# Kernel tuning notes

Measured on AMD Instinct MI355X. Metric: run time of the kernel, lower is better.

## Reference

```python
import jax, jax.numpy as jnp
import numpy as np

EPS = 1e-5


def _bn(x, gamma, beta, mean, var):
    # Inference-mode BatchNorm2d over channel dim (NCHW -> axis 1).
    inv = gamma / jnp.sqrt(var + EPS)
    return x * inv[None, :, None, None] + (beta - mean * inv)[None, :, None, None]


def setup_inputs() -> dict:
    key = jax.random.key(0)
    ks = jax.random.split(key, 6)
    N, Cin, Cout, T, V = 64, 64, 128, 300, 25
    x = jax.random.normal(ks[0], (N, Cin, T, V), dtype=jnp.float32)
    A = jax.random.uniform(ks[1], (V, V), dtype=jnp.float32)  # fixed adjacency (non-trainable buffer)
    edge = jnp.ones((V, V), dtype=jnp.float32)                # learnable edge mask, init ones
    gcn_w = jax.random.normal(ks[2], (Cout, Cin), dtype=jnp.float32) * 0.05
    gcn_b = jnp.zeros((Cout,), dtype=jnp.float32)
    res_w = jax.random.normal(ks[3], (Cout, Cin), dtype=jnp.float32) * 0.05
    res_b = jnp.zeros((Cout,), dtype=jnp.float32)
    return {
        'x': x, 'A': A, 'edge': edge,
        'gcn_w': gcn_w, 'gcn_b': gcn_b,
        'bn_gamma': jnp.ones((Cout,), jnp.float32), 'bn_beta': jnp.zeros((Cout,), jnp.float32),
        'bn_mean': jnp.zeros((Cout,), jnp.float32), 'bn_var': jnp.ones((Cout,), jnp.float32),
        'res_w': res_w, 'res_b': res_b,
        'rbn_gamma': jnp.ones((Cout,), jnp.float32), 'rbn_beta': jnp.zeros((Cout,), jnp.float32),
        'rbn_mean': jnp.zeros((Cout,), jnp.float32), 'rbn_var': jnp.ones((Cout,), jnp.float32),
    }


def reference(x, A, edge, gcn_w, gcn_b, bn_gamma, bn_beta, bn_mean, bn_var,
              res_w, res_b, rbn_gamma, rbn_beta, rbn_mean, rbn_var):
    # x: [N, Cin, T, V]
    # residual branch: 1x1 conv + BN (in_channel != out_channel path)
    res = jnp.einsum('oc,nctv->notv', res_w, x) + res_b[None, :, None, None]
    res = _bn(res, rbn_gamma, rbn_beta, rbn_mean, rbn_var)
    # main branch: 1x1 conv -> adjacency einsum -> BN
    y = jnp.einsum('oc,nctv->notv', gcn_w, x) + gcn_b[None, :, None, None]
    y = jnp.einsum('nctv,vw->nctw', y, A * edge)
    y = _bn(y, bn_gamma, bn_beta, bn_mean, bn_var)
    # keep_prob = 1.0 -> Randomized_DropBlock_Ske / DropBlockT_1d are identity
    return jax.nn.relu(y + res)
```

## Files before the change

kernel.cpp:

```cpp
#include <hip/hip_runtime.h>
#include <stdint.h>

#define N_ 64
#define C_ 64
#define O_ 128
#define T_ 300
#define V_ 25
#define TB 4
#define JB (TB * 32)
#define KB 128
#define LDB 136

typedef __attribute__((ext_vector_type(8))) short short8;
typedef __attribute__((ext_vector_type(4))) float floatx4;

__device__ __forceinline__ short f2bf(float f) {
  unsigned u = __float_as_uint(f);
  unsigned r = (u + 0x7FFFu + ((u >> 16) & 1u)) >> 16;
  return (short)(r & 0xFFFFu);
}

__global__ void sgc_prep(const float* __restrict__ A, const float* __restrict__ edge,
                         const float* __restrict__ gcn_w, const float* __restrict__ gcn_b,
                         const float* __restrict__ bn_g, const float* __restrict__ bn_b,
                         const float* __restrict__ bn_m, const float* __restrict__ bn_v,
                         const float* __restrict__ res_w, const float* __restrict__ res_b,
                         const float* __restrict__ rg, const float* __restrict__ rb,
                         const float* __restrict__ rm, const float* __restrict__ rv,
                         short* __restrict__ Wcat, float* __restrict__ M2p,
                         float* __restrict__ Cwp) {
  const int tid = threadIdx.x;
  for (int i = tid; i < 25 * 32; i += 256) {
    const int v = i >> 5, w = i & 31;
    M2p[i] = (w < 25) ? A[v * 25 + w] * edge[v * 25 + w] : 0.f;
  }
  for (int i = tid; i < O_ * 32; i += 256) {
    const int o = i >> 5, w = i & 31;
    const float inv1 = bn_g[o] * rsqrtf(bn_v[o] + 1e-5f);
    const float inv2 = rg[o] * rsqrtf(rv[o] + 1e-5f);
    float S = 0.f;
    if (w < 25) {
      for (int v = 0; v < 25; ++v) S += A[v * 25 + w] * edge[v * 25 + w];
    }
    Cwp[i] = inv1 * gcn_b[o] * S + (bn_b[o] - bn_m[o] * inv1) + inv2 * res_b[o] +
             (rb[o] - rm[o] * inv2);
  }
  for (int i = tid; i < O_ * KB; i += 256) {
    const int o = i >> 7, k = i & 127;
    const float inv1 = bn_g[o] * rsqrtf(bn_v[o] + 1e-5f);
    const float inv2 = rg[o] * rsqrtf(rv[o] + 1e-5f);
    const float val = (k < 64) ? inv2 * res_w[o * 64 + k] : inv1 * gcn_w[o * 64 + (k - 64)];
    Wcat[i] = f2bf(val);
  }
}

__global__ __launch_bounds__(256, 2) void sgc_main(const float* __restrict__ x,
                                                   const short* __restrict__ Wcat,
                                                   const float* __restrict__ M2p,
                                                   const float* __restrict__ Cw,
                                                   float* __restrict__ out) {
  __shared__ short Bs[JB * LDB];
  const int tid = threadIdx.x;
  const int b = blockIdx.x;
  const int n = b / 75;
  const int t0 = (b % 75) * TB;

  {
    const int tl = tid >> 6;
    const int c = tid & 63;
    const float* xrow = x + (((n * C_ + c) * T_) + (t0 + tl)) * V_;
    float xr[25];
#pragma unroll
    for (int v = 0; v < 25; ++v) xr[v] = xrow[v];
#pragma unroll
    for (int v = 0; v < 25; ++v) Bs[(tl * 32 + v) * LDB + c] = f2bf(xr[v]);
#pragma unroll
    for (int v = 25; v < 32; ++v) {
      Bs[(tl * 32 + v) * LDB + c] = 0;
      Bs[(tl * 32 + v) * LDB + 64 + c] = 0;
    }
    float xa[25];
#pragma unroll
    for (int w = 0; w < 25; ++w) xa[w] = 0.f;
    for (int v = 0; v < 25; ++v) {
      const float xv = xr[v];
      const float* m2 = M2p + v * 32;
#pragma unroll
      for (int w = 0; w < 25; ++w) xa[w] = __builtin_fmaf(xv, m2[w], xa[w]);
    }
#pragma unroll
    for (int w = 0; w < 25; ++w) Bs[(tl * 32 + w) * LDB + 64 + c] = f2bf(xa[w]);
  }
  __syncthreads();

  const int lane = tid & 63;
  const int wv = tid >> 6;
  const int l15 = lane & 15;
  const int quad = lane >> 4;
  const int obase = wv * 32;

  short8 af[2][4];
#pragma unroll
  for (int mt = 0; mt < 2; ++mt) {
#pragma unroll
    for (int kq = 0; kq < 4; ++kq) {
      af[mt][kq] =
          *(const short8*)(Wcat + (obase + mt * 16 + l15) * KB + kq * 32 + quad * 8);
    }
  }

  floatx4 acc[2][8];
#pragma unroll
  for (int mt = 0; mt < 2; ++mt)
#pragma unroll
    for (int jt = 0; jt < 8; ++jt) acc[mt][jt] = (floatx4){0.f, 0.f, 0.f, 0.f};

#pragma unroll
  for (int jt = 0; jt < 8; ++jt) {
#pragma unroll
    for (int kq = 0; kq < 4; ++kq) {
      const short8 bf =
          *(const short8*)(&Bs[(jt * 16 + l15) * LDB + kq * 32 + quad * 8]);
      acc[0][jt] = __builtin_amdgcn_mfma_f32_16x16x32_bf16(af[0][kq], bf, acc[0][jt], 0, 0, 0);
      acc[1][jt] = __builtin_amdgcn_mfma_f32_16x16x32_bf16(af[1][kq], bf, acc[1][jt], 0, 0, 0);
    }
  }

#pragma unroll
  for (int mt = 0; mt < 2; ++mt) {
#pragma unroll
    for (int jt = 0; jt < 8; ++jt) {
      const int j = jt * 16 + l15;
      const int w = j & 31;
      if (w < 25) {
        const int tloc = j >> 5;
        const int o0 = obase + mt * 16 + quad * 4;
        float* op = out + (((n * O_ + o0) * T_) + (t0 + tloc)) * V_ + w;
        const float* cwp = Cw + o0 * 32 + w;
#pragma unroll
        for (int r = 0; r < 4; ++r) {
          const float val = acc[mt][jt][r] + cwp[r * 32];
          op[r * (T_ * V_)] = val > 0.f ? val : 0.f;
        }
      }
    }
  }
}

extern "C" void kernel_launch(void* const* d_in, const int* in_sizes, int n_in,
                              void* d_out, int out_size, void* d_ws, size_t ws_size,
                              hipStream_t stream) {
  const float* x = (const float*)d_in[0];
  const float* A = (const float*)d_in[1];
  const float* edge = (const float*)d_in[2];
  const float* gcn_w = (const float*)d_in[3];
  const float* gcn_b = (const float*)d_in[4];
  const float* bn_g = (const float*)d_in[5];
  const float* bn_b = (const float*)d_in[6];
  const float* bn_m = (const float*)d_in[7];
  const float* bn_v = (const float*)d_in[8];
  const float* res_w = (const float*)d_in[9];
  const float* res_b = (const float*)d_in[10];
  const float* rg = (const float*)d_in[11];
  const float* rb = (const float*)d_in[12];
  const float* rm = (const float*)d_in[13];
  const float* rv = (const float*)d_in[14];

  char* ws = (char*)d_ws;
  short* Wcat = (short*)(ws);
  float* M2p = (float*)(ws + 32768);
  float* Cwp = (float*)(ws + 36864);
  float* out = (float*)d_out;

  hipLaunchKernelGGL(sgc_prep, dim3(1), dim3(256), 0, stream, A, edge, gcn_w, gcn_b,
                     bn_g, bn_b, bn_m, bn_v, res_w, res_b, rg, rb, rm, rv, Wcat, M2p, Cwp);
  hipLaunchKernelGGL(sgc_main, dim3(N_ * (T_ / TB)), dim3(256), 0, stream, x, Wcat, M2p,
                     Cwp, out);
}
```

Measured before the change: 475.0 us.

## Stage x loads and output stores through LDS for coalesced vector access

```diff
diff --git a/kernel.cpp b/kernel.cpp
--- a/kernel.cpp
+++ b/kernel.cpp
@@ -10,6 +10,10 @@
 #define JB (TB * 32)
 #define KB 128
 #define LDB 136
+#define SXS 65
+#define BS_OFF 26000
+#define SMEM_BYTES (BS_OFF + JB * LDB * 2)
+#define STW 3200
 
 typedef __attribute__((ext_vector_type(8))) short short8;
 typedef __attribute__((ext_vector_type(4))) float floatx4;
@@ -59,40 +63,14 @@
                                                    const float* __restrict__ M2p,
                                                    const float* __restrict__ Cw,
                                                    float* __restrict__ out) {
-  __shared__ short Bs[JB * LDB];
+  __shared__ __align__(16) char smem[SMEM_BYTES];
+  float* const xs = (float*)smem;
+  short* const Bs = (short*)(smem + BS_OFF);
+
   const int tid = threadIdx.x;
   const int b = blockIdx.x;
   const int n = b / 75;
   const int t0 = (b % 75) * TB;
-
-  {
-    const int tl = tid >> 6;
-    const int c = tid & 63;
-    const float* xrow = x + (((n * C_ + c) * T_) + (t0 + tl)) * V_;
-    float xr[25];
-#pragma unroll
-    for (int v = 0; v < 25; ++v) xr[v] = xrow[v];
-#pragma unroll
-    for (int v = 0; v < 25; ++v) Bs[(tl * 32 + v) * LDB + c] = f2bf(xr[v]);
-#pragma unroll
-    for (int v = 25; v < 32; ++v) {
-      Bs[(tl * 32 + v) * LDB + c] = 0;
-      Bs[(tl * 32 + v) * LDB + 64 + c] = 0;
-    }
-    float xa[25];
-#pragma unroll
-    for (int w = 0; w < 25; ++w) xa[w] = 0.f;
-    for (int v = 0; v < 25; ++v) {
-      const float xv = xr[v];
-      const float* m2 = M2p + v * 32;
-#pragma unroll
-      for (int w = 0; w < 25; ++w) xa[w] = __builtin_fmaf(xv, m2[w], xa[w]);
-    }
-#pragma unroll
-    for (int w = 0; w < 25; ++w) Bs[(tl * 32 + w) * LDB + 64 + c] = f2bf(xa[w]);
-  }
-  __syncthreads();
-
   const int lane = tid & 63;
   const int wv = tid >> 6;
   const int l15 = lane & 15;
@@ -109,6 +87,48 @@
     }
   }
 
+  {
+    const float* xbase = x + n * (C_ * T_ * V_) + t0 * V_;
+    for (int u = tid; u < 1600; u += 256) {
+      const int c = u / 25;
+      const int q = u - c * 25;
+      const floatx4 vv = *(const floatx4*)(xbase + c * (T_ * V_) + q * 4);
+      const int a0 = (q * 4) * SXS + c;
+#pragma unroll
+      for (int i = 0; i < 4; ++i) xs[a0 + i * SXS] = vv[i];
+    }
+    for (int u = tid; u < 448; u += 256) {
+      const int row = u >> 4;
+      const int col = u & 15;
+      const int tl = row / 7;
+      const int v = 25 + (row - tl * 7);
+      *(floatx4*)(Bs + (tl * 32 + v) * LDB + col * 8) = (floatx4){0.f, 0.f, 0.f, 0.f};
+    }
+  }
+  __syncthreads();
+
+  {
+    const int tl = wv;
+    const int c = lane;
+    float xr[25];
+#pragma unroll
+    for (int v = 0; v < 25; ++v) xr[v] = xs[(tl * 25 + v) * SXS + c];
+#pragma unroll
+    for (int v = 0; v < 25; ++v) Bs[(tl * 32 + v) * LDB + c] = f2bf(xr[v]);
+    float xa[25];
+#pragma unroll
+    for (int w = 0; w < 25; ++w) xa[w] = 0.f;
+    for (int v = 0; v < 25; ++v) {
+      const float xv = xr[v];
+      const float* m2 = M2p + v * 32;
+#pragma unroll
+      for (int w = 0; w < 25; ++w) xa[w] = __builtin_fmaf(xv, m2[w], xa[w]);
+    }
+#pragma unroll
+    for (int w = 0; w < 25; ++w) Bs[(tl * 32 + w) * LDB + 64 + c] = f2bf(xa[w]);
+  }
+  __syncthreads();
+
   floatx4 acc[2][8];
 #pragma unroll
   for (int mt = 0; mt < 2; ++mt)
@@ -125,24 +145,39 @@
       acc[1][jt] = __builtin_amdgcn_mfma_f32_16x16x32_bf16(af[1][kq], bf, acc[1][jt], 0, 0, 0);
     }
   }
-
-#pragma unroll
-  for (int mt = 0; mt < 2; ++mt) {
-#pragma unroll
-    for (int jt = 0; jt < 8; ++jt) {
-      const int j = jt * 16 + l15;
-      const int w = j & 31;
-      if (w < 25) {
-        const int tloc = j >> 5;
-        const int o0 = obase + mt * 16 + quad * 4;
-        float* op = out + (((n * O_ + o0) * T_) + (t0 + tloc)) * V_ + w;
-        const float* cwp = Cw + o0 * 32 + w;
-#pragma unroll
-        for (int r = 0; r < 4; ++r) {
-          const float val = acc[mt][jt][r] + cwp[r * 32];
-          op[r * (T_ * V_)] = val > 0.f ? val : 0.f;
+  __syncthreads();
+
+  {
+    float* const st = (float*)smem + wv * STW;
+#pragma unroll
+    for (int mt = 0; mt < 2; ++mt) {
+#pragma unroll
+      for (int jt = 0; jt < 8; ++jt) {
+        const int j = jt * 16 + l15;
+        const int w = j & 31;
+        if (w < 25) {
+          const int tloc = j >> 5;
+          const int ol0 = mt * 16 + quad * 4;
+          const float* cwp = Cw + (obase + ol0) * 32 + w;
+          float* sp = st + ol0 * 100 + tloc * 25 + w;
+#pragma unroll
+          for (int r = 0; r < 4; ++r) {
+            const float val = acc[mt][jt][r] + cwp[r * 32];
+            sp[r * 100] = val > 0.f ? val : 0.f;
+          }
         }
       }
+    }
+  }
+  __syncthreads();
+
+  {
+    float* const st = (float*)smem + wv * STW;
+    float* const ob = out + ((n * O_ + obase) * T_ + t0) * V_;
+    for (int u = lane; u < 800; u += 64) {
+      const int ol = u / 25;
+      const int q = u - ol * 25;
+      *(floatx4*)(ob + ol * (T_ * V_) + q * 4) = *(const floatx4*)(st + ol * 100 + q * 4);
     }
   }
 }
```

New measurement: 528.1 us. +11.2%, slower.

## Compute x·M2 adjacency product with split-bf16 MFMA instead of scalar FMAs

Applied to the files above, without the earlier changes.

```diff
diff --git a/kernel.cpp b/kernel.cpp
--- a/kernel.cpp
+++ b/kernel.cpp
@@ -19,6 +19,9 @@
   unsigned r = (u + 0x7FFFu + ((u >> 16) & 1u)) >> 16;
   return (short)(r & 0xFFFFu);
 }
+__device__ __forceinline__ float bf2f(short h) {
+  return __uint_as_float(((unsigned)(unsigned short)h) << 16);
+}
 
 __global__ void sgc_prep(const float* __restrict__ A, const float* __restrict__ edge,
                          const float* __restrict__ gcn_w, const float* __restrict__ gcn_b,
@@ -27,12 +30,19 @@
                          const float* __restrict__ res_w, const float* __restrict__ res_b,
                          const float* __restrict__ rg, const float* __restrict__ rb,
                          const float* __restrict__ rm, const float* __restrict__ rv,
-                         short* __restrict__ Wcat, float* __restrict__ M2p,
+                         short* __restrict__ Wcat, short* __restrict__ M2f,
                          float* __restrict__ Cwp) {
   const int tid = threadIdx.x;
-  for (int i = tid; i < 25 * 32; i += 256) {
-    const int v = i >> 5, w = i & 31;
-    M2p[i] = (w < 25) ? A[v * 25 + w] * edge[v * 25 + w] : 0.f;
+  for (int i = tid; i < 2048; i += 256) {
+    const int wh = i >> 10;
+    const int hl = (i >> 9) & 1;
+    const int ln = (i >> 3) & 63;
+    const int jj = i & 7;
+    const int v = ((ln >> 4) << 3) + jj;
+    const int w = wh * 16 + (ln & 15);
+    float m = (v < 25 && w < 25) ? A[v * 25 + w] * edge[v * 25 + w] : 0.f;
+    const short h = f2bf(m);
+    M2f[i] = hl ? f2bf(m - bf2f(h)) : h;
   }
   for (int i = tid; i < O_ * 32; i += 256) {
     const int o = i >> 5, w = i & 31;
@@ -54,45 +64,16 @@
   }
 }
 
-__global__ __launch_bounds__(256, 2) void sgc_main(const float* __restrict__ x,
+__global__ __launch_bounds__(256, 3) void sgc_main(const float* __restrict__ x,
                                                    const short* __restrict__ Wcat,
-                                                   const float* __restrict__ M2p,
+                                                   const short* __restrict__ M2f,
                                                    const float* __restrict__ Cw,
                                                    float* __restrict__ out) {
-  __shared__ short Bs[JB * LDB];
+  __shared__ __align__(16) short Bs[JB * LDB];
   const int tid = threadIdx.x;
   const int b = blockIdx.x;
   const int n = b / 75;
   const int t0 = (b % 75) * TB;
-
-  {
-    const int tl = tid >> 6;
-    const int c = tid & 63;
-    const float* xrow = x + (((n * C_ + c) * T_) + (t0 + tl)) * V_;
-    float xr[25];
-#pragma unroll
-    for (int v = 0; v < 25; ++v) xr[v] = xrow[v];
-#pragma unroll
-    for (int v = 0; v < 25; ++v) Bs[(tl * 32 + v) * LDB + c] = f2bf(xr[v]);
-#pragma unroll
-    for (int v = 25; v < 32; ++v) {
-      Bs[(tl * 32 + v) * LDB + c] = 0;
-      Bs[(tl * 32 + v) * LDB + 64 + c] = 0;
-    }
-    float xa[25];
-#pragma unroll
-    for (int w = 0; w < 25; ++w) xa[w] = 0.f;
-    for (int v = 0; v < 25; ++v) {
-      const float xv = xr[v];
-      const float* m2 = M2p + v * 32;
-#pragma unroll
-      for (int w = 0; w < 25; ++w) xa[w] = __builtin_fmaf(xv, m2[w], xa[w]);
-    }
-#pragma unroll
-    for (int w = 0; w < 25; ++w) Bs[(tl * 32 + w) * LDB + 64 + c] = f2bf(xa[w]);
-  }
-  __syncthreads();
-
   const int lane = tid & 63;
   const int wv = tid >> 6;
   const int l15 = lane & 15;
@@ -108,6 +89,66 @@
           *(const short8*)(Wcat + (obase + mt * 16 + l15) * KB + kq * 32 + quad * 8);
     }
   }
+
+  {
+    const int t = wv;
+    const short8 m2hi0 = *(const short8*)(M2f + ((0 * 2 + 0) * 64 + lane) * 8);
+    const short8 m2lo0 = *(const short8*)(M2f + ((0 * 2 + 1) * 64 + lane) * 8);
+    const short8 m2hi1 = *(const short8*)(M2f + ((1 * 2 + 0) * 64 + lane) * 8);
+    const short8 m2lo1 = *(const short8*)(M2f + ((1 * 2 + 1) * 64 + lane) * 8);
+
+    short8 xhi[4], xlo[4];
+    const float* xq = x + ((n * C_ + l15) * T_ + (t0 + t)) * V_ + quad * 8;
+#pragma unroll
+    for (int ct = 0; ct < 4; ++ct) {
+      const float* xp = xq + ct * 16 * (T_ * V_);
+      float xv[8];
+      if (quad < 3) {
+#pragma unroll
+        for (int i = 0; i < 8; ++i) xv[i] = xp[i];
+      } else {
+        xv[0] = xp[0];
+#pragma unroll
+        for (int i = 1; i < 8; ++i) xv[i] = 0.f;
+      }
+      short8 h, l;
+#pragma unroll
+      for (int i = 0; i < 8; ++i) {
+        const short hb = f2bf(xv[i]);
+        h[i] = hb;
+        l[i] = f2bf(xv[i] - bf2f(hb));
+      }
+      xhi[ct] = h;
+      xlo[ct] = l;
+      short* bp = Bs + (t * 32 + quad * 8) * LDB + ct * 16 + l15;
+      if (quad < 3) {
+#pragma unroll
+        for (int i = 0; i < 8; ++i) bp[i * LDB] = h[i];
+      } else {
+        bp[0] = h[0];
+      }
+    }
+
+#pragma unroll
+    for (int ct = 0; ct < 4; ++ct) {
+#pragma unroll
+      for (int wh = 0; wh < 2; ++wh) {
+        floatx4 a = (floatx4){0.f, 0.f, 0.f, 0.f};
+        a = __builtin_amdgcn_mfma_f32_16x16x32_bf16(xhi[ct], wh ? m2hi1 : m2hi0, a, 0, 0, 0);
+        a = __builtin_amdgcn_mfma_f32_16x16x32_bf16(xlo[ct], wh ? m2hi1 : m2hi0, a, 0, 0, 0);
+        a = __builtin_amdgcn_mfma_f32_16x16x32_bf16(xhi[ct], wh ? m2lo1 : m2lo0, a, 0, 0, 0);
+        const unsigned d0 = ((unsigned)(unsigned short)f2bf(a[1]) << 16) |
+                            (unsigned short)f2bf(a[0]);
+        const unsigned d1 = ((unsigned)(unsigned short)f2bf(a[3]) << 16) |
+                            (unsigned short)f2bf(a[2]);
+        unsigned* wp =
+            (unsigned*)(Bs + (t * 32 + wh * 16 + l15) * LDB + 64 + ct * 16 + quad * 4);
+        wp[0] = d0;
+        wp[1] = d1;
+      }
+    }
+  }
+  __syncthreads();
 
   floatx4 acc[2][8];
 #pragma unroll
@@ -168,12 +209,12 @@
 
   char* ws = (char*)d_ws;
   short* Wcat = (short*)(ws);
-  float* M2p = (float*)(ws + 32768);
+  short* M2f = (short*)(ws + 32768);
   float* Cwp = (float*)(ws + 36864);
   float* out = (float*)d_out;
 
   hipLaunchKernelGGL(sgc_prep, dim3(1), dim3(256), 0, stream, A, edge, gcn_w, gcn_b,
-                     bn_g, bn_b, bn_m, bn_v, res_w, res_b, rg, rb, rm, rv, Wcat, M2p, Cwp);
-  hipLaunchKernelGGL(sgc_main, dim3(N_ * (T_ / TB)), dim3(256), 0, stream, x, Wcat, M2p,
+                     bn_g, bn_b, bn_m, bn_v, res_w, res_b, rg, rb, rm, rv, Wcat, M2f, Cwp);
+  hipLaunchKernelGGL(sgc_main, dim3(N_ * (T_ / TB)), dim3(256), 0, stream, x, Wcat, M2f,
                      Cwp, out);
 }
```

New measurement: 489.0 us. 2.9% more time.
